# Optimization experiments

Hardware: AMD Instinct MI355X
Metric: run time of the kernel (lower is better)

Reference implementation:

```python
import jax, jax.numpy as jnp
import numpy as np

VOCAB = 4101
NUM_IGNORED = 5  # token ids {0,1,2,3,4} are ignored


def _calc_frequency(x):
    # x: [N, L] int token ids -> [N, VOCAB] scaled frequency vectors
    n = x.shape[0]
    hist = jnp.zeros((n, VOCAB), dtype=jnp.float32)
    hist = hist.at[jnp.arange(n)[:, None], x].add(1.0)  # batched bincount
    hist = hist.at[:, :NUM_IGNORED].set(0.0)            # drop ignored tokens
    seq_len = hist.sum(axis=-1, keepdims=True)          # count of kept tokens
    return jnp.where(seq_len > 0, hist / seq_len * 10.0, hist)


def _mlp(h, W1, b1, W2, b2):
    h = jax.nn.relu(h @ W1 + b1)
    return h @ W2 + b2


def setup_inputs() -> dict:
    key = jax.random.key(0)
    k1, k2, k3 = jax.random.split(key, 3)
    B, L = 1024, 4096
    X = jax.random.randint(k1, (B, 3, L), 0, VOCAB, dtype=jnp.int64)
    W1 = jax.random.normal(k2, (VOCAB, 768), dtype=jnp.float32) * 0.02
    b1 = jnp.zeros((768,), dtype=jnp.float32)
    W2 = jax.random.normal(k3, (768, 256), dtype=jnp.float32) * 0.02
    b2 = jnp.zeros((256,), dtype=jnp.float32)
    return {"X": X, "W1": W1, "b1": b1, "W2": W2, "b2": b2}


def reference(X, W1, b1, W2, b2):
    B, three, L = X.shape
    flat = X.reshape(B * three, L)          # process anchor/pos/neg together
    freq = _calc_frequency(flat)            # [3B, VOCAB]
    out = _mlp(freq, W1, b1, W2, b2)        # [3B, 256]
    out = out.reshape(B, three, 256)
    return (out[:, 0], out[:, 1], out[:, 2])
```

## Files before the change

### kernel.cpp

```cpp
#include <hip/hip_runtime.h>

typedef unsigned short ushort_t;
typedef __bf16 bf16_8 __attribute__((ext_vector_type(8)));
typedef float f32x4 __attribute__((ext_vector_type(4)));

#define VOCAB 4101
#define KPAD  4224
#define NROWS 3072
#define HDIM  768
#define ODIM  256


static __device__ __forceinline__ unsigned short f2bf(float f) {
  unsigned int u = __float_as_uint(f);
  unsigned int r = (u + 0x7fffu + ((u >> 16) & 1u)) >> 16;
  return (unsigned short)r;
}

static __device__ __forceinline__ void async_copy16(const void* g, void* l) {
  __builtin_amdgcn_global_load_lds(
      (const __attribute__((address_space(1))) void*)g,
      (__attribute__((address_space(3))) void*)l, 16, 0, 0);
}


__global__ __launch_bounds__(256)
void prep_kernel(const int* __restrict__ X,
                 const float* __restrict__ W1,
                 const float* __restrict__ W2,
                 ushort_t* __restrict__ A,
                 ushort_t* __restrict__ W1T,
                 ushort_t* __restrict__ W2T,
                 float* __restrict__ scales) {
  __shared__ __align__(16) unsigned char smem[16896];
  const int bid = blockIdx.x;

  if (bid < NROWS) {
    unsigned int* h = (unsigned int*)smem;
    const int r = bid;
    uint4* h4 = (uint4*)smem;
    for (int i = threadIdx.x; i < 1056; i += 256)
      h4[i] = (uint4){0u, 0u, 0u, 0u};
    __syncthreads();

    const int4* xp = reinterpret_cast<const int4*>(X + (size_t)r * 4096);
    #pragma unroll
    for (int i = 0; i < 4; ++i) {
      int4 v = xp[i * 256 + threadIdx.x];
      atomicAdd(&h[v.x], 1u);
      atomicAdd(&h[v.y], 1u);
      atomicAdd(&h[v.z], 1u);
      atomicAdd(&h[v.w], 1u);
    }
    __syncthreads();

    const unsigned int ignored = h[0] + h[1] + h[2] + h[3] + h[4];
    const float s = 10.0f / (float)(4096u - ignored);
    if (threadIdx.x == 0) scales[r] = s;

    uint4* Ar4 = (uint4*)(A + (size_t)r * KPAD);
    for (int i = threadIdx.x; i < 528; i += 256) {
      const int b0 = i * 8;
      unsigned int w[4];
      #pragma unroll
      for (int j = 0; j < 4; ++j) {
        int ia = b0 + 2 * j, ib = b0 + 2 * j + 1;
        unsigned int ca = (ia >= 5 && ia < VOCAB) ? h[ia] : 0u;
        unsigned int cb = (ib >= 5 && ib < VOCAB) ? h[ib] : 0u;
        w[j] = (unsigned int)f2bf((float)ca) | ((unsigned int)f2bf((float)cb) << 16);
      }
      Ar4[i] = (uint4){w[0], w[1], w[2], w[3]};
    }
  } else {
    ushort_t (*tile)[65] = (ushort_t(*)[65])smem;
    const float* src; ushort_t* dst;
    int K, N, Kpad, kb, nb;
    if (bid < NROWS + 792) {
      const int t = bid - NROWS;
      src = W1; dst = W1T; K = VOCAB; N = HDIM; Kpad = KPAD;
      kb = (t % 66) * 64; nb = (t / 66) * 64;
    } else {
      const int t = bid - NROWS - 792;
      src = W2; dst = W2T; K = HDIM; N = ODIM; Kpad = HDIM;
      kb = (t % 12) * 64; nb = (t / 12) * 64;
    }
    const int tr = threadIdx.x >> 6;
    const int tc = threadIdx.x & 63;
    #pragma unroll
    for (int i = 0; i < 16; ++i) {
      int r = i * 4 + tr;
      int k = kb + r;
      float v = (k < K) ? src[(size_t)k * N + nb + tc] : 0.0f;
      tile[r][tc] = f2bf(v);
    }
    __syncthreads();
    #pragma unroll
    for (int i = 0; i < 16; ++i) {
      int r = i * 4 + tr;
      dst[(size_t)(nb + r) * Kpad + kb + tc] = tile[tc][r];
    }
  }
}


__global__ __launch_bounds__(128)
void gemm1_fused(const ushort_t* __restrict__ A, int lda,
                 const ushort_t* __restrict__ Bt, int ldb,
                 int ktiles,
                 const float* __restrict__ scales,
                 const float* __restrict__ bias,
                 ushort_t* __restrict__ H) {
  __shared__ __align__(16) ushort_t Alds[2][96 * 128];
  __shared__ __align__(16) ushort_t Blds[2][48 * 128];
  const int tid  = threadIdx.x;
  const int lane = tid & 63;
  const int wv   = tid >> 6;
  const int m0   = blockIdx.x * 96;
  const int n0   = blockIdx.y * 48;

  f32x4 acc[3][3];
  #pragma unroll
  for (int m = 0; m < 3; ++m)
    #pragma unroll
    for (int n = 0; n < 3; ++n)
      acc[m][n] = (f32x4){0.f, 0.f, 0.f, 0.f};

#define STAGE(bi, kt)                                                          \
  {                                                                            \
    const int k0_ = (kt) * 128;                                                \
    _Pragma("unroll")                                                          \
    for (int i = 0; i < 12; ++i) {                                             \
      const int cd  = i * 128 + tid;                                           \
      const int row = cd >> 4;                                                 \
      const int cc  = (cd & 15) ^ (row & 7);                                   \
      async_copy16(A + (size_t)(m0 + row) * lda + k0_ + cc * 8,                \
                   (char*)&Alds[bi][0] + cd * 16);                             \
    }                                                                          \
    _Pragma("unroll")                                                          \
    for (int i = 0; i < 6; ++i) {                                              \
      const int cd  = i * 128 + tid;                                           \
      const int row = cd >> 4;                                                 \
      const int cc  = (cd & 15) ^ (row & 7);                                   \
      async_copy16(Bt + (size_t)(n0 + row) * ldb + k0_ + cc * 8,               \
                   (char*)&Blds[bi][0] + cd * 16);                             \
    }                                                                          \
  }

  STAGE(0, 0);
  __syncthreads();

  int cur = 0;
  for (int t = 0; t < ktiles; ++t) {
    if (t + 1 < ktiles) STAGE(cur ^ 1, t + 1);
    const int hi = lane >> 4;
    #pragma unroll
    for (int kk = 0; kk < 4; ++kk) {
      bf16_8 af[3], bf[3];
      #pragma unroll
      for (int m = 0; m < 3; ++m) {
        const int ra = wv * 48 + m * 16 + (lane & 15);
        const int ca = kk * 4 + hi;
        af[m] = *(const bf16_8*)((const char*)&Alds[cur][0] +
                                 (ra * 16 + (ca ^ (ra & 7))) * 16);
      }
      #pragma unroll
      for (int n = 0; n < 3; ++n) {
        const int rb = n * 16 + (lane & 15);
        const int cb = kk * 4 + hi;
        bf[n] = *(const bf16_8*)((const char*)&Blds[cur][0] +
                                 (rb * 16 + (cb ^ (rb & 7))) * 16);
      }
      #pragma unroll
      for (int m = 0; m < 3; ++m)
        #pragma unroll
        for (int n = 0; n < 3; ++n)
          acc[m][n] = __builtin_amdgcn_mfma_f32_16x16x32_bf16(af[m], bf[n],
                                                              acc[m][n], 0, 0, 0);
    }
    __syncthreads();
    cur ^= 1;
  }
#undef STAGE

  const int rbase = (lane >> 4) * 4;
  const int cf    = lane & 15;
  #pragma unroll
  for (int m = 0; m < 3; ++m) {
    #pragma unroll
    for (int n = 0; n < 3; ++n) {
      #pragma unroll
      for (int reg = 0; reg < 4; ++reg) {
        const int gr = m0 + wv * 48 + m * 16 + rbase + reg;
        const int gc = n0 + n * 16 + cf;
        float v = fmaxf(acc[m][n][reg] * scales[gr] + bias[gc], 0.0f);
        H[(size_t)gr * HDIM + gc] = f2bf(v);
      }
    }
  }
}


__global__ __launch_bounds__(384)
void gemm2_fused(const ushort_t* __restrict__ A, int lda,
                 const ushort_t* __restrict__ Bt, int ldb,
                 int ktiles,
                 const float* __restrict__ bias,
                 float* __restrict__ outp) {
  __shared__ __align__(16) ushort_t Alds[2][96 * 128];
  __shared__ __align__(16) ushort_t Blds[2][32 * 128];
  const int tid  = threadIdx.x;
  const int lane = tid & 63;
  const int wv   = tid >> 6;
  const int m0   = blockIdx.x * 96;
  const int n0   = blockIdx.y * 32;

  f32x4 acc[2];
  acc[0] = (f32x4){0.f, 0.f, 0.f, 0.f};
  acc[1] = (f32x4){0.f, 0.f, 0.f, 0.f};

#define STAGE(bi, kt)                                                          \
  {                                                                            \
    const int k0_ = (kt) * 128;                                                \
    _Pragma("unroll")                                                          \
    for (int i = 0; i < 4; ++i) {                                              \
      const int cd  = i * 384 + tid;                                           \
      const int row = cd >> 4;                                                 \
      const int cc  = (cd & 15) ^ (row & 7);                                   \
      async_copy16(A + (size_t)(m0 + row) * lda + k0_ + cc * 8,                \
                   (char*)&Alds[bi][0] + cd * 16);                             \
    }                                                                          \
    {                                                                          \
      const int cd  = tid;                                                     \
      const int row = cd >> 4;                                                 \
      const int cc  = (cd & 15) ^ (row & 7);                                   \
      async_copy16(Bt + (size_t)(n0 + row) * ldb + k0_ + cc * 8,               \
                   (char*)&Blds[bi][0] + cd * 16);                             \
    }                                                                          \
    if (tid < 128) {                                                           \
      const int cd  = 384 + tid;                                               \
      const int row = cd >> 4;                                                 \
      const int cc  = (cd & 15) ^ (row & 7);                                   \
      async_copy16(Bt + (size_t)(n0 + row) * ldb + k0_ + cc * 8,               \
                   (char*)&Blds[bi][0] + cd * 16);                             \
    }                                                                          \
  }

  STAGE(0, 0);
  __syncthreads();

  int cur = 0;
  for (int t = 0; t < ktiles; ++t) {
    if (t + 1 < ktiles) STAGE(cur ^ 1, t + 1);
    const int hi = lane >> 4;
    #pragma unroll
    for (int kk = 0; kk < 4; ++kk) {
      bf16_8 af, bf[2];
      {
        const int ra = wv * 16 + (lane & 15);
        const int ca = kk * 4 + hi;
        af = *(const bf16_8*)((const char*)&Alds[cur][0] +
                              (ra * 16 + (ca ^ (ra & 7))) * 16);
      }
      #pragma unroll
      for (int n = 0; n < 2; ++n) {
        const int rb = n * 16 + (lane & 15);
        const int cb = kk * 4 + hi;
        bf[n] = *(const bf16_8*)((const char*)&Blds[cur][0] +
                                 (rb * 16 + (cb ^ (rb & 7))) * 16);
      }
      #pragma unroll
      for (int n = 0; n < 2; ++n)
        acc[n] = __builtin_amdgcn_mfma_f32_16x16x32_bf16(af, bf[n], acc[n], 0, 0, 0);
    }
    __syncthreads();
    cur ^= 1;
  }
#undef STAGE

  const int rbase = (lane >> 4) * 4;
  const int cf    = lane & 15;
  #pragma unroll
  for (int n = 0; n < 2; ++n) {
    #pragma unroll
    for (int reg = 0; reg < 4; ++reg) {
      const int gr = m0 + wv * 16 + rbase + reg;
      const int gc = n0 + n * 16 + cf;
      float v = acc[n][reg] + bias[gc];
      outp[(size_t)(gr % 3) * (1024 * ODIM) + (size_t)(gr / 3) * ODIM + gc] = v;
    }
  }
}


extern "C" void kernel_launch(void* const* d_in, const int* in_sizes, int n_in,
                              void* d_out, int out_size, void* d_ws, size_t ws_size,
                              hipStream_t stream) {
  const int*   X  = (const int*)d_in[0];
  const float* W1 = (const float*)d_in[1];
  const float* b1 = (const float*)d_in[2];
  const float* W2 = (const float*)d_in[3];
  const float* b2 = (const float*)d_in[4];
  float* out = (float*)d_out;

  char* ws = (char*)d_ws;
  ushort_t* A      = (ushort_t*)(ws);
  ushort_t* W1T    = (ushort_t*)(ws + 25952256);
  ushort_t* H      = (ushort_t*)(ws + 32440320);
  ushort_t* W2T    = (ushort_t*)(ws + 37158912);
  float*    scales = (float*)   (ws + 37552128);

  prep_kernel<<<NROWS + 792 + 48, 256, 0, stream>>>(X, W1, W2, A, W1T, W2T, scales);

  gemm1_fused<<<dim3(NROWS / 96, HDIM / 48), 128, 0, stream>>>(
      A, KPAD, W1T, KPAD, KPAD / 128, scales, b1, H);

  gemm2_fused<<<dim3(NROWS / 96, ODIM / 32), 384, 0, stream>>>(
      H, HDIM, W2T, HDIM, HDIM / 128, b2, out);
}
```

Baseline: 67.35 us.

## Load GEMM1 A fragments directly to registers and widen block to 96x96 tile

New measurement: 106.9 us. +58.8%, slower.

```diff
diff --git a/kernel.cpp b/kernel.cpp
--- a/kernel.cpp
+++ b/kernel.cpp
@@ -103,20 +103,27 @@
 }
 
 
-__global__ __launch_bounds__(128)
+__global__ __launch_bounds__(256)
 void gemm1_fused(const ushort_t* __restrict__ A, int lda,
                  const ushort_t* __restrict__ Bt, int ldb,
                  int ktiles,
                  const float* __restrict__ scales,
                  const float* __restrict__ bias,
                  ushort_t* __restrict__ H) {
-  __shared__ __align__(16) ushort_t Alds[2][96 * 128];
-  __shared__ __align__(16) ushort_t Blds[2][48 * 128];
+  __shared__ __align__(16) ushort_t Blds[2][96 * 128];
   const int tid  = threadIdx.x;
   const int lane = tid & 63;
   const int wv   = tid >> 6;
+  const int wrow = wv >> 1;
+  const int wcol = wv & 1;
   const int m0   = blockIdx.x * 96;
-  const int n0   = blockIdx.y * 48;
+  const int n0   = blockIdx.y * 96;
+
+  const ushort_t* pA[3];
+  #pragma unroll
+  for (int m = 0; m < 3; ++m)
+    pA[m] = A + (size_t)(m0 + wrow * 48 + m * 16 + (lane & 15)) * lda +
+            (lane >> 4) * 8;
 
   f32x4 acc[3][3];
   #pragma unroll
@@ -129,16 +136,8 @@
   {                                                                            \
     const int k0_ = (kt) * 128;                                                \
     _Pragma("unroll")                                                          \
-    for (int i = 0; i < 12; ++i) {                                             \
-      const int cd  = i * 128 + tid;                                           \
-      const int row = cd >> 4;                                                 \
-      const int cc  = (cd & 15) ^ (row & 7);                                   \
-      async_copy16(A + (size_t)(m0 + row) * lda + k0_ + cc * 8,                \
-                   (char*)&Alds[bi][0] + cd * 16);                             \
-    }                                                                          \
-    _Pragma("unroll")                                                          \
     for (int i = 0; i < 6; ++i) {                                              \
-      const int cd  = i * 128 + tid;                                           \
+      const int cd  = i * 256 + tid;                                           \
       const int row = cd >> 4;                                                 \
       const int cc  = (cd & 15) ^ (row & 7);                                   \
       async_copy16(Bt + (size_t)(n0 + row) * ldb + k0_ + cc * 8,               \
@@ -151,21 +150,22 @@
 
   int cur = 0;
   for (int t = 0; t < ktiles; ++t) {
+    bf16_8 areg[4][3];
+    #pragma unroll
+    for (int kk = 0; kk < 4; ++kk)
+      #pragma unroll
+      for (int m = 0; m < 3; ++m)
+        areg[kk][m] = *(const bf16_8*)(pA[m] + t * 128 + kk * 32);
+
     if (t + 1 < ktiles) STAGE(cur ^ 1, t + 1);
+
     const int hi = lane >> 4;
     #pragma unroll
     for (int kk = 0; kk < 4; ++kk) {
-      bf16_8 af[3], bf[3];
-      #pragma unroll
-      for (int m = 0; m < 3; ++m) {
-        const int ra = wv * 48 + m * 16 + (lane & 15);
-        const int ca = kk * 4 + hi;
-        af[m] = *(const bf16_8*)((const char*)&Alds[cur][0] +
-                                 (ra * 16 + (ca ^ (ra & 7))) * 16);
-      }
+      bf16_8 bf[3];
       #pragma unroll
       for (int n = 0; n < 3; ++n) {
-        const int rb = n * 16 + (lane & 15);
+        const int rb = wcol * 48 + n * 16 + (lane & 15);
         const int cb = kk * 4 + hi;
         bf[n] = *(const bf16_8*)((const char*)&Blds[cur][0] +
                                  (rb * 16 + (cb ^ (rb & 7))) * 16);
@@ -174,7 +174,7 @@
       for (int m = 0; m < 3; ++m)
         #pragma unroll
         for (int n = 0; n < 3; ++n)
-          acc[m][n] = __builtin_amdgcn_mfma_f32_16x16x32_bf16(af[m], bf[n],
+          acc[m][n] = __builtin_amdgcn_mfma_f32_16x16x32_bf16(areg[kk][m], bf[n],
                                                               acc[m][n], 0, 0, 0);
     }
     __syncthreads();
@@ -190,8 +190,8 @@
     for (int n = 0; n < 3; ++n) {
       #pragma unroll
       for (int reg = 0; reg < 4; ++reg) {
-        const int gr = m0 + wv * 48 + m * 16 + rbase + reg;
-        const int gc = n0 + n * 16 + cf;
+        const int gr = m0 + wrow * 48 + m * 16 + rbase + reg;
+        const int gc = n0 + wcol * 48 + n * 16 + cf;
         float v = fmaxf(acc[m][n][reg] * scales[gr] + bias[gc], 0.0f);
         H[(size_t)gr * HDIM + gc] = f2bf(v);
       }
@@ -311,7 +311,7 @@
 
   prep_kernel<<<NROWS + 792 + 48, 256, 0, stream>>>(X, W1, W2, A, W1T, W2T, scales);
 
-  gemm1_fused<<<dim3(NROWS / 96, HDIM / 48), 128, 0, stream>>>(
+  gemm1_fused<<<dim3(NROWS / 96, HDIM / 96), 256, 0, stream>>>(
       A, KPAD, W1T, KPAD, KPAD / 128, scales, b1, H);
 
   gemm2_fused<<<dim3(NROWS / 96, ODIM / 32), 384, 0, stream>>>(
```
